# Optimization experiments

Measured on AMD Instinct MI355X. Metric: run time of the kernel, lower is better.

Reference implementation:

```python
import jax, jax.numpy as jnp
import numpy as np

B, S, D = 2, 2048, 2048      # batch, seq, hidden_dim
F = 4096                      # expert ffn dim
E, K = 8, 2                   # num_experts, top_k


def setup_inputs() -> dict:
    key = jax.random.key(0)
    k0, k1, k2, k3, k4 = jax.random.split(key, 5)
    sc_d = 1.0 / np.sqrt(D)
    sc_f = 1.0 / np.sqrt(F)
    return {
        "hidden_states": jax.random.normal(k0, (B, S, D), jnp.float32),
        "gate_w": jax.random.normal(k1, (E, D), jnp.float32) * sc_d,  # router Linear(D->E)
        "w1": jax.random.normal(k2, (E, F, D), jnp.float32) * sc_d,   # stacked expert w1
        "w2": jax.random.normal(k3, (E, D, F), jnp.float32) * sc_f,   # stacked expert w2
        "w3": jax.random.normal(k4, (E, F, D), jnp.float32) * sc_d,   # stacked expert w3
    }


def reference(hidden_states, gate_w, w1, w2, w3):
    b, s, d = hidden_states.shape
    x = hidden_states.reshape(-1, d)                    # [T, D]
    T = x.shape[0]

    # Router: softmax in float32, top-k, renormalize (matches torch code)
    logits = x @ gate_w.T                               # [T, E]
    probs = jax.nn.softmax(logits.astype(jnp.float32), axis=-1)
    top_w, top_e = jax.lax.top_k(probs, K)              # [T, K]
    top_w = top_w / jnp.sum(top_w, axis=-1, keepdims=True)
    top_w = top_w.astype(x.dtype)

    # Scatter top-k weights into dense per-expert weight matrix [T, E]
    rows = jnp.arange(T)[:, None]
    w_full = jnp.zeros((T, E), x.dtype).at[rows, top_e].set(top_w)

    # Expert SwiGLU MLPs; dense-per-expert with zero weight for unrouted tokens
    # is mathematically identical to the gather/scatter loop in the original.
    y = jnp.zeros_like(x)
    for e in range(E):
        h = jax.nn.silu(x @ w1[e].T) * (x @ w3[e].T)    # [T, F]
        y = y + w_full[:, e:e + 1] * (h @ w2[e].T)      # [T, D]

    return y.reshape(b, s, d)
```

## Files before the change

kernel.cpp:

```cpp
#include <hip/hip_runtime.h>
#include <hip/hip_bf16.h>

#define TTOK 4096
#define DIM  2048
#define FF   4096
#define NE   8
#define TROWS 8192

#define BM 256
#define BK 64

typedef __attribute__((ext_vector_type(4))) float  f32x4;
typedef __attribute__((ext_vector_type(8))) short  s16x8;
typedef __attribute__((ext_vector_type(8))) unsigned short u16x8;

__device__ __forceinline__ unsigned short f2bf(float f) {
  union { __hip_bfloat16 h; unsigned short u; } cv;
  cv.h = __float2bfloat16(f);
  return cv.u;
}
__device__ __forceinline__ float bf2f(unsigned short u) {
  union { unsigned int i; float f; } cv;
  cv.i = ((unsigned int)u) << 16;
  return cv.f;
}

__device__ __forceinline__ void gl_lds16(const void* g, void* s) {
  __builtin_amdgcn_global_load_lds(
      (__attribute__((address_space(1))) void*)(g),
      (__attribute__((address_space(3))) void*)(s), 16, 0, 0);
}

#define VMW(NN) asm volatile("s_waitcnt vmcnt(" #NN ")" ::: "memory")

__global__ __launch_bounds__(256) void cvt_kernel(const float* __restrict__ s,
                                                  unsigned short* __restrict__ d, int n8) {
  int i = blockIdx.x * 256 + threadIdx.x;
  if (i >= n8) return;
  f32x4 v0 = *(const f32x4*)(s + (size_t)i * 8);
  f32x4 v1 = *(const f32x4*)(s + (size_t)i * 8 + 4);
  u16x8 o;
#pragma unroll
  for (int j = 0; j < 4; ++j) { o[j] = f2bf(v0[j]); o[j + 4] = f2bf(v1[j]); }
  *(u16x8*)(d + (size_t)i * 8) = o;
}

__global__ void router_kernel(const float* __restrict__ x,
                              const float* __restrict__ gate_w,
                              int* __restrict__ tope, float* __restrict__ topw,
                              int* __restrict__ counts) {
  const int t = blockIdx.x;
  const int tid = threadIdx.x;
  const float* xr = x + (size_t)t * DIM;
  float p[NE];
#pragma unroll
  for (int e = 0; e < NE; ++e) p[e] = 0.f;
  for (int d = tid; d < DIM; d += 256) {
    float xv = xr[d];
#pragma unroll
    for (int e = 0; e < NE; ++e) p[e] += xv * gate_w[e * DIM + d];
  }
#pragma unroll
  for (int off = 32; off > 0; off >>= 1) {
#pragma unroll
    for (int e = 0; e < NE; ++e) p[e] += __shfl_down(p[e], off);
  }
  __shared__ float red[4][NE];
  const int wid = tid >> 6, lane = tid & 63;
  if (lane == 0) {
#pragma unroll
    for (int e = 0; e < NE; ++e) red[wid][e] = p[e];
  }
  __syncthreads();
  if (tid == 0) {
    float l[NE];
#pragma unroll
    for (int e = 0; e < NE; ++e) l[e] = red[0][e] + red[1][e] + red[2][e] + red[3][e];
    float mx = l[0];
#pragma unroll
    for (int e = 1; e < NE; ++e) mx = fmaxf(mx, l[e]);
    float pr[NE]; float sum = 0.f;
#pragma unroll
    for (int e = 0; e < NE; ++e) { pr[e] = __expf(l[e] - mx); sum += pr[e]; }
    float inv = 1.f / sum;
#pragma unroll
    for (int e = 0; e < NE; ++e) pr[e] *= inv;
    int i0 = 0; float p0 = pr[0];
#pragma unroll
    for (int e = 1; e < NE; ++e) if (pr[e] > p0) { p0 = pr[e]; i0 = e; }
    int i1 = -1; float p1 = -1.f;
#pragma unroll
    for (int e = 0; e < NE; ++e) if (e != i0 && pr[e] > p1) { p1 = pr[e]; i1 = e; }
    float wsum = p0 + p1;
    tope[t * 2 + 0] = i0; topw[t * 2 + 0] = p0 / wsum;
    tope[t * 2 + 1] = i1; topw[t * 2 + 1] = p1 / wsum;
    atomicAdd(&counts[i0], 1);
    atomicAdd(&counts[i1], 1);
  }
}

__global__ void prefix_kernel(const int* __restrict__ counts, int* __restrict__ basep) {
  if (threadIdx.x == 0 && blockIdx.x == 0) {
    int acc = 0;
    for (int e = 0; e < NE; ++e) { basep[e] = acc; acc += counts[e]; }
  }
}

__global__ void fill_kernel(const int* __restrict__ tope, const float* __restrict__ topw,
                            const int* __restrict__ basep, int* __restrict__ fillp,
                            int* __restrict__ rowtok, float* __restrict__ roww,
                            int* __restrict__ rowof) {
  int t = blockIdx.x * blockDim.x + threadIdx.x;
  if (t >= TTOK) return;
#pragma unroll
  for (int s = 0; s < 2; ++s) {
    int e = tope[t * 2 + s];
    int r = basep[e] + atomicAdd(&fillp[e], 1);
    rowtok[r] = t;
    roww[r] = topw[t * 2 + s];
    rowof[t * 2 + s] = r;
  }
}

template <int MODE, int K, int N>
__global__ __launch_bounds__(512, 1) void gemm8(
    const unsigned short* __restrict__ Asrc, const unsigned short* __restrict__ Bw,
    const int* __restrict__ rowtok, const float* __restrict__ roww,
    const int* __restrict__ counts, const int* __restrict__ basep,
    void* __restrict__ Out) {
  const int e = blockIdx.z;
  const int cnt = counts[e];
  const int m0 = blockIdx.y * BM;
  if (m0 >= cnt) return;
  const int n0 = blockIdx.x * BM;
  const int base_e = basep[e];

  __shared__ unsigned short As[2][BM * BK];
  __shared__ unsigned short Bs[2][BM * BK];

  const int tid = threadIdx.x;
  const int lane = tid & 63;
  const int w = tid >> 6;
  const int wm = w >> 2;
  const int wn = w & 3;

  const int lsub  = lane >> 3;
  const int lslot = lane & 7;
  const int swz_e = 8 * (lslot ^ lsub);

  const unsigned short* pA[4];
  const unsigned short* pB[4];
#pragma unroll
  for (int s = 0; s < 4; ++s) {
    int rl = s * 64 + w * 8 + lsub;
    int ga = m0 + rl; if (ga > cnt - 1) ga = cnt - 1;
    if (MODE == 0) {
      int tok = rowtok[base_e + ga];
      pA[s] = Asrc + (size_t)tok * K + swz_e;
    } else {
      pA[s] = Asrc + (size_t)(base_e + ga) * K + swz_e;
    }
    pB[s] = Bw + ((size_t)e * N + n0 + s * 64 + w * 8 + lsub) * K + swz_e;
  }

  const int frow = lane & 15;
  const int klane = lane >> 4;
  const int ks0 = (klane * 8) ^ ((frow & 7) * 8);
  const int ks1 = (32 + klane * 8) ^ ((frow & 7) * 8);

  f32x4 acc[8][4];
#pragma unroll
  for (int mf = 0; mf < 8; ++mf)
#pragma unroll
    for (int nf = 0; nf < 4; ++nf) acc[mf][nf] = (f32x4)0.f;

#define ST_A(BUF, G0, T) do { \
    gl_lds16(pA[G0]     + (size_t)(T) * BK, &As[BUF][((G0) * 64 + w * 8) * BK]); \
    gl_lds16(pA[(G0)+1] + (size_t)(T) * BK, &As[BUF][(((G0)+1) * 64 + w * 8) * BK]); \
  } while (0)
#define ST_B(BUF, G0, T) do { \
    gl_lds16(pB[G0]     + (size_t)(T) * BK, &Bs[BUF][((G0) * 64 + w * 8) * BK]); \
    gl_lds16(pB[(G0)+1] + (size_t)(T) * BK, &Bs[BUF][(((G0)+1) * 64 + w * 8) * BK]); \
  } while (0)

#define RD_A(MH, BUF) do { \
    _Pragma("unroll") \
    for (int ii = 0; ii < 4; ++ii) { \
      a[ii][0] = *(const s16x8*)&As[BUF][(wm * 128 + (MH) * 64 + ii * 16 + frow) * BK + ks0]; \
      a[ii][1] = *(const s16x8*)&As[BUF][(wm * 128 + (MH) * 64 + ii * 16 + frow) * BK + ks1]; \
    } } while (0)
#define RD_B(DST, NH, BUF) do { \
    _Pragma("unroll") \
    for (int j = 0; j < 2; ++j) { \
      DST[j][0] = *(const s16x8*)&Bs[BUF][(wn * 64 + (NH) * 32 + j * 16 + frow) * BK + ks0]; \
      DST[j][1] = *(const s16x8*)&Bs[BUF][(wn * 64 + (NH) * 32 + j * 16 + frow) * BK + ks1]; \
    } } while (0)

#define MM(MH, NH, BB) do { \
    __builtin_amdgcn_s_setprio(1); \
    _Pragma("unroll") \
    for (int ii = 0; ii < 4; ++ii) \
      _Pragma("unroll") \
      for (int j = 0; j < 2; ++j) { \
        acc[(MH) * 4 + ii][(NH) * 2 + j] = __builtin_amdgcn_mfma_f32_16x16x32_bf16( \
            a[ii][0], BB[j][0], acc[(MH) * 4 + ii][(NH) * 2 + j], 0, 0, 0); \
        acc[(MH) * 4 + ii][(NH) * 2 + j] = __builtin_amdgcn_mfma_f32_16x16x32_bf16( \
            a[ii][1], BB[j][1], acc[(MH) * 4 + ii][(NH) * 2 + j], 0, 0, 0); \
      } \
    __builtin_amdgcn_s_setprio(0); \
  } while (0)

#define MIDSYNC do { \
    __builtin_amdgcn_sched_barrier(0); \
    __builtin_amdgcn_s_barrier(); \
    asm volatile("s_waitcnt lgkmcnt(0)" ::: "memory"); \
    __builtin_amdgcn_sched_barrier(0); \
  } while (0)
#define ENDB do { \
    __builtin_amdgcn_sched_barrier(0); \
    __builtin_amdgcn_s_barrier(); \
  } while (0)

  const int NT = K / BK;

  ST_A(0, 0, 0); ST_A(0, 2, 0);
  ST_B(0, 0, 0); ST_B(0, 2, 0);
  ST_B(1, 0, 1); ST_B(1, 2, 1);
  VMW(4);
  __builtin_amdgcn_s_barrier();

  s16x8 a[4][2], bl[2][2], bh[2][2];

  for (int t = 0; t < NT; t += 2) {
    const bool full = (t + 2 < NT);

    RD_A(0, 0); RD_B(bl, 0, 0);
    ST_A(1, 0, t + 1);
    MIDSYNC; MM(0, 0, bl); ENDB;

    RD_B(bh, 1, 0);
    ST_A(1, 2, t + 1);
    MIDSYNC; MM(0, 1, bh); ENDB;

    RD_A(1, 0);
    if (full) ST_B(0, 0, t + 2);
    MIDSYNC; MM(1, 1, bh); ENDB;

    if (full) ST_B(0, 2, t + 2);
    MIDSYNC; MM(1, 0, bl);
    if (full) { VMW(4); } else { VMW(0); }
    ENDB;

    RD_A(0, 1); RD_B(bl, 0, 1);
    if (full) ST_A(0, 0, t + 2);
    MIDSYNC; MM(0, 0, bl); ENDB;

    RD_B(bh, 1, 1);
    if (full) ST_A(0, 2, t + 2);
    MIDSYNC; MM(0, 1, bh); ENDB;

    RD_A(1, 1);
    if (full) ST_B(1, 0, t + 3);
    MIDSYNC; MM(1, 1, bh); ENDB;

    if (full) ST_B(1, 2, t + 3);
    MIDSYNC; MM(1, 0, bl);
    if (full) { VMW(4); }
    ENDB;
  }
#undef ST_A
#undef ST_B
#undef RD_A
#undef RD_B
#undef MM
#undef MIDSYNC
#undef ENDB

#pragma unroll
  for (int mf = 0; mf < 8; ++mf) {
#pragma unroll
    for (int nf = 0; nf < 4; ++nf) {
      int col = n0 + wn * 64 + nf * 16 + frow;
#pragma unroll
      for (int j = 0; j < 4; ++j) {
        int rl = wm * 128 + (mf >> 2) * 64 + (mf & 3) * 16 + klane * 4 + j;
        int grow = m0 + rl;
        if (grow < cnt) {
          if (MODE == 0) {
            ((unsigned short*)Out)[(size_t)(base_e + grow) * N + col] = f2bf(acc[mf][nf][j]);
          } else {
            float wv = roww[base_e + grow];
            ((float*)Out)[(size_t)(base_e + grow) * N + col] = acc[mf][nf][j] * wv;
          }
        }
      }
    }
  }
}

__global__ __launch_bounds__(256) void swiglu_kernel(const unsigned short* __restrict__ h1,
                                                     const unsigned short* __restrict__ h3,
                                                     unsigned short* __restrict__ H, int n8) {
  int i = blockIdx.x * 256 + threadIdx.x;
  if (i >= n8) return;
  u16x8 v1 = *(const u16x8*)(h1 + (size_t)i * 8);
  u16x8 v3 = *(const u16x8*)(h3 + (size_t)i * 8);
  u16x8 o;
#pragma unroll
  for (int j = 0; j < 8; ++j) {
    float s = bf2f(v1[j]);
    float g = bf2f(v3[j]);
    o[j] = f2bf((s / (1.f + __expf(-s))) * g);
  }
  *(u16x8*)(H + (size_t)i * 8) = o;
}

__global__ __launch_bounds__(256) void combine_kernel(const float* __restrict__ R,
                                                      const int* __restrict__ rowof,
                                                      float* __restrict__ y) {
  int idx = blockIdx.x * 256 + threadIdx.x;
  int t = idx >> 9;
  int d4 = idx & 511;
  int r0 = rowof[t * 2], r1 = rowof[t * 2 + 1];
  f32x4 a = *(const f32x4*)(R + (size_t)r0 * DIM + d4 * 4);
  f32x4 b = *(const f32x4*)(R + (size_t)r1 * DIM + d4 * 4);
  *(f32x4*)(y + (size_t)t * DIM + d4 * 4) = a + b;
}

extern "C" void kernel_launch(void* const* d_in, const int* in_sizes, int n_in,
                              void* d_out, int out_size, void* d_ws, size_t ws_size,
                              hipStream_t stream) {
  const float* x      = (const float*)d_in[0];
  const float* gate_w = (const float*)d_in[1];
  const float* w1     = (const float*)d_in[2];
  const float* w2     = (const float*)d_in[3];
  const float* w3     = (const float*)d_in[4];
  float* y = (float*)d_out;

  char* ws = (char*)d_ws;
  const size_t MB = 1ull << 20;
  int*   tope   = (int*)(ws);
  float* topw   = (float*)(ws + (32 << 10));
  int*   rowtok = (int*)(ws + (64 << 10));
  float* roww   = (float*)(ws + (96 << 10));
  int*   rowof  = (int*)(ws + (128 << 10));
  int*   counts = (int*)(ws + (160 << 10));
  int*   basep  = counts + 32;
  int*   fillp  = counts + 64;

  unsigned short* xb  = (unsigned short*)(ws + 1 * MB);
  unsigned short* H1  = (unsigned short*)(ws + 17 * MB);
  unsigned short* H3  = (unsigned short*)(ws + 81 * MB);
  unsigned short* w1b = (unsigned short*)(ws + 145 * MB);
  unsigned short* w3b = (unsigned short*)(ws + 273 * MB);
  unsigned short* w2b = (unsigned short*)(ws + 401 * MB);
  float*          R   = (float*)(ws + 145 * MB);

  hipMemsetAsync(counts, 0, 512, stream);
  router_kernel<<<TTOK, 256, 0, stream>>>(x, gate_w, tope, topw, counts);
  prefix_kernel<<<1, 64, 0, stream>>>(counts, basep);
  fill_kernel<<<TTOK / 256, 256, 0, stream>>>(tope, topw, basep, fillp, rowtok, roww, rowof);

  const int nw8 = NE * FF * DIM / 8;
  const int nx8 = TTOK * DIM / 8;
  cvt_kernel<<<nw8 / 256, 256, 0, stream>>>(w1, w1b, nw8);
  cvt_kernel<<<nw8 / 256, 256, 0, stream>>>(w3, w3b, nw8);
  cvt_kernel<<<nw8 / 256, 256, 0, stream>>>(w2, w2b, nw8);
  cvt_kernel<<<nx8 / 256, 256, 0, stream>>>(x, xb, nx8);

  gemm8<0, DIM, FF><<<dim3(FF / BM, 16, NE), 512, 0, stream>>>(
      xb, w1b, rowtok, roww, counts, basep, (void*)H1);
  gemm8<0, DIM, FF><<<dim3(FF / BM, 16, NE), 512, 0, stream>>>(
      xb, w3b, rowtok, roww, counts, basep, (void*)H3);
  swiglu_kernel<<<TROWS * FF / 8 / 256, 256, 0, stream>>>(H1, H3, H1, TROWS * FF / 8);
  gemm8<1, FF, DIM><<<dim3(DIM / BM, 16, NE), 512, 0, stream>>>(
      H1, w2b, rowtok, roww, counts, basep, (void*)R);
  combine_kernel<<<TTOK * DIM / 4 / 256, 256, 0, stream>>>(R, rowof, y);
}
```

Measured before the change: 986.4 us.

## Fuse w1/w3 GEMMs with SwiGLU epilogue and remap workgroups across experts

Replaces the two separate up-projection GEMMs and the standalone SwiGLU kernel with one kernel. It loads a shared A tile once, computes both w1 and w3 accumulators over 128-wide N tiles, and applies SiLU*gate in the epilogue. This removes the H3 intermediate write/read and re-reading the gathered activations twice. It also adds a block-index remapping that interleaves experts across consecutive workgroups to balance load, at the cost of a narrower N tile per block.

```diff
diff --git a/kernel.cpp b/kernel.cpp
--- a/kernel.cpp
+++ b/kernel.cpp
@@ -32,6 +32,17 @@
 }
 
 #define VMW(NN) asm volatile("s_waitcnt vmcnt(" #NN ")" ::: "memory")
+
+#define MIDSYNC do { \
+    __builtin_amdgcn_sched_barrier(0); \
+    __builtin_amdgcn_s_barrier(); \
+    asm volatile("s_waitcnt lgkmcnt(0)" ::: "memory"); \
+    __builtin_amdgcn_sched_barrier(0); \
+  } while (0)
+#define ENDB do { \
+    __builtin_amdgcn_sched_barrier(0); \
+    __builtin_amdgcn_s_barrier(); \
+  } while (0)
 
 __global__ __launch_bounds__(256) void cvt_kernel(const float* __restrict__ s,
                                                   unsigned short* __restrict__ d, int n8) {
@@ -122,21 +133,28 @@
   }
 }
 
-template <int MODE, int K, int N>
-__global__ __launch_bounds__(512, 1) void gemm8(
-    const unsigned short* __restrict__ Asrc, const unsigned short* __restrict__ Bw,
-    const int* __restrict__ rowtok, const float* __restrict__ roww,
+__global__ __launch_bounds__(512, 1) void gemm1f(
+    const unsigned short* __restrict__ xb, const unsigned short* __restrict__ w1b,
+    const unsigned short* __restrict__ w3b, const int* __restrict__ rowtok,
     const int* __restrict__ counts, const int* __restrict__ basep,
-    void* __restrict__ Out) {
-  const int e = blockIdx.z;
+    unsigned short* __restrict__ H) {
+  constexpr int GX = FF / 128;
+  constexpr int GY = TTOK / BM;
+  constexpr int Q  = GX * GY;
+  int lin = (blockIdx.z * GY + blockIdx.y) * GX + blockIdx.x;
+  int wg = (lin & 7) * Q + (lin >> 3);
+  const int e   = wg / (GX * GY);
+  const int rem = wg % (GX * GY);
+  const int m0  = (rem / GX) * BM;
+  const int n0  = (rem % GX) * 128;
+
   const int cnt = counts[e];
-  const int m0 = blockIdx.y * BM;
   if (m0 >= cnt) return;
-  const int n0 = blockIdx.x * BM;
   const int base_e = basep[e];
 
   __shared__ unsigned short As[2][BM * BK];
-  __shared__ unsigned short Bs[2][BM * BK];
+  __shared__ unsigned short B1s[2][128 * BK];
+  __shared__ unsigned short B3s[2][128 * BK];
 
   const int tid = threadIdx.x;
   const int lane = tid & 63;
@@ -149,18 +167,181 @@
   const int swz_e = 8 * (lslot ^ lsub);
 
   const unsigned short* pA[4];
-  const unsigned short* pB[4];
+  const unsigned short* pB1[2];
+  const unsigned short* pB3[2];
 #pragma unroll
   for (int s = 0; s < 4; ++s) {
     int rl = s * 64 + w * 8 + lsub;
     int ga = m0 + rl; if (ga > cnt - 1) ga = cnt - 1;
-    if (MODE == 0) {
-      int tok = rowtok[base_e + ga];
-      pA[s] = Asrc + (size_t)tok * K + swz_e;
-    } else {
-      pA[s] = Asrc + (size_t)(base_e + ga) * K + swz_e;
+    int tok = rowtok[base_e + ga];
+    pA[s] = xb + (size_t)tok * DIM + swz_e;
+  }
+#pragma unroll
+  for (int s = 0; s < 2; ++s) {
+    int rl = s * 64 + w * 8 + lsub;
+    pB1[s] = w1b + ((size_t)e * FF + n0 + rl) * DIM + swz_e;
+    pB3[s] = w3b + ((size_t)e * FF + n0 + rl) * DIM + swz_e;
+  }
+
+  const int frow = lane & 15;
+  const int klane = lane >> 4;
+  const int ks0 = (klane * 8) ^ ((frow & 7) * 8);
+  const int ks1 = (32 + klane * 8) ^ ((frow & 7) * 8);
+
+  f32x4 acc1[8][2], acc3[8][2];
+#pragma unroll
+  for (int mf = 0; mf < 8; ++mf)
+#pragma unroll
+    for (int nf = 0; nf < 2; ++nf) { acc1[mf][nf] = (f32x4)0.f; acc3[mf][nf] = (f32x4)0.f; }
+
+#define ST_A(BUF, G0, T) do { \
+    gl_lds16(pA[G0]     + (size_t)(T) * BK, &As[BUF][((G0) * 64 + w * 8) * BK]); \
+    gl_lds16(pA[(G0)+1] + (size_t)(T) * BK, &As[BUF][(((G0)+1) * 64 + w * 8) * BK]); \
+  } while (0)
+#define ST_B1(BUF, T) do { \
+    gl_lds16(pB1[0] + (size_t)(T) * BK, &B1s[BUF][(0  + w * 8) * BK]); \
+    gl_lds16(pB1[1] + (size_t)(T) * BK, &B1s[BUF][(64 + w * 8) * BK]); \
+  } while (0)
+#define ST_B3(BUF, T) do { \
+    gl_lds16(pB3[0] + (size_t)(T) * BK, &B3s[BUF][(0  + w * 8) * BK]); \
+    gl_lds16(pB3[1] + (size_t)(T) * BK, &B3s[BUF][(64 + w * 8) * BK]); \
+  } while (0)
+
+#define RD_A(MH, BUF) do { \
+    _Pragma("unroll") \
+    for (int ii = 0; ii < 4; ++ii) { \
+      a[ii][0] = *(const s16x8*)&As[BUF][(wm * 128 + (MH) * 64 + ii * 16 + frow) * BK + ks0]; \
+      a[ii][1] = *(const s16x8*)&As[BUF][(wm * 128 + (MH) * 64 + ii * 16 + frow) * BK + ks1]; \
+    } } while (0)
+#define RD_BX(DST, ARR, BUF) do { \
+    _Pragma("unroll") \
+    for (int j = 0; j < 2; ++j) { \
+      DST[j][0] = *(const s16x8*)&ARR[BUF][(wn * 32 + j * 16 + frow) * BK + ks0]; \
+      DST[j][1] = *(const s16x8*)&ARR[BUF][(wn * 32 + j * 16 + frow) * BK + ks1]; \
+    } } while (0)
+
+#define MMX(ACC, MH, BB) do { \
+    __builtin_amdgcn_s_setprio(1); \
+    _Pragma("unroll") \
+    for (int ii = 0; ii < 4; ++ii) \
+      _Pragma("unroll") \
+      for (int j = 0; j < 2; ++j) { \
+        ACC[(MH) * 4 + ii][j] = __builtin_amdgcn_mfma_f32_16x16x32_bf16( \
+            a[ii][0], BB[j][0], ACC[(MH) * 4 + ii][j], 0, 0, 0); \
+        ACC[(MH) * 4 + ii][j] = __builtin_amdgcn_mfma_f32_16x16x32_bf16( \
+            a[ii][1], BB[j][1], ACC[(MH) * 4 + ii][j], 0, 0, 0); \
+      } \
+    __builtin_amdgcn_s_setprio(0); \
+  } while (0)
+
+  const int NT = DIM / BK;
+
+  ST_A(0, 0, 0); ST_A(0, 2, 0);
+  ST_B1(0, 0); ST_B3(0, 0);
+  ST_B1(1, 1); ST_B3(1, 1);
+  VMW(4);
+  __builtin_amdgcn_s_barrier();
+
+  s16x8 a[4][2], bl[2][2], bh[2][2];
+
+  for (int t = 0; t < NT; t += 2) {
+    const bool full = (t + 2 < NT);
+
+    RD_A(0, 0); RD_BX(bl, B1s, 0);
+    ST_A(1, 0, t + 1);
+    MIDSYNC; MMX(acc1, 0, bl); ENDB;
+    RD_BX(bh, B3s, 0);
+    ST_A(1, 2, t + 1);
+    MIDSYNC; MMX(acc3, 0, bh); ENDB;
+    RD_A(1, 0);
+    if (full) ST_B1(0, t + 2);
+    MIDSYNC; MMX(acc3, 1, bh); ENDB;
+    if (full) ST_B3(0, t + 2);
+    MIDSYNC; MMX(acc1, 1, bl);
+    if (full) { VMW(4); } else { VMW(0); }
+    ENDB;
+
+    RD_A(0, 1); RD_BX(bl, B1s, 1);
+    if (full) ST_A(0, 0, t + 2);
+    MIDSYNC; MMX(acc1, 0, bl); ENDB;
+    RD_BX(bh, B3s, 1);
+    if (full) ST_A(0, 2, t + 2);
+    MIDSYNC; MMX(acc3, 0, bh); ENDB;
+    RD_A(1, 1);
+    if (full) ST_B1(1, t + 3);
+    MIDSYNC; MMX(acc3, 1, bh); ENDB;
+    if (full) ST_B3(1, t + 3);
+    MIDSYNC; MMX(acc1, 1, bl);
+    if (full) { VMW(4); }
+    ENDB;
+  }
+#undef ST_A
+#undef ST_B1
+#undef ST_B3
+#undef RD_A
+#undef RD_BX
+#undef MMX
+
+#pragma unroll
+  for (int mf = 0; mf < 8; ++mf) {
+#pragma unroll
+    for (int nf = 0; nf < 2; ++nf) {
+      int col = n0 + wn * 32 + nf * 16 + frow;
+      f32x4 c1 = acc1[mf][nf], c3 = acc3[mf][nf];
+#pragma unroll
+      for (int j = 0; j < 4; ++j) {
+        int rl = wm * 128 + (mf >> 2) * 64 + (mf & 3) * 16 + klane * 4 + j;
+        int grow = m0 + rl;
+        if (grow < cnt) {
+          float s = c1[j];
+          float hval = (s / (1.f + __expf(-s))) * c3[j];
+          H[(size_t)(base_e + grow) * FF + col] = f2bf(hval);
+        }
+      }
     }
-    pB[s] = Bw + ((size_t)e * N + n0 + s * 64 + w * 8 + lsub) * K + swz_e;
+  }
+}
+
+template <int K, int N>
+__global__ __launch_bounds__(512, 1) void gemm8(
+    const unsigned short* __restrict__ Asrc, const unsigned short* __restrict__ Bw,
+    const float* __restrict__ roww, const int* __restrict__ counts,
+    const int* __restrict__ basep, float* __restrict__ Out) {
+  constexpr int GX = N / BM;
+  constexpr int GY = TTOK / BM;
+  constexpr int Q  = GX * GY;
+  int lin = (blockIdx.z * GY + blockIdx.y) * GX + blockIdx.x;
+  int wg = (lin & 7) * Q + (lin >> 3);
+  const int e   = wg / (GX * GY);
+  const int rem = wg % (GX * GY);
+  const int m0  = (rem / GX) * BM;
+  const int n0  = (rem % GX) * BM;
+
+  const int cnt = counts[e];
+  if (m0 >= cnt) return;
+  const int base_e = basep[e];
+
+  __shared__ unsigned short As[2][BM * BK];
+  __shared__ unsigned short Bs[2][BM * BK];
+
+  const int tid = threadIdx.x;
+  const int lane = tid & 63;
+  const int w = tid >> 6;
+  const int wm = w >> 2;
+  const int wn = w & 3;
+
+  const int lsub  = lane >> 3;
+  const int lslot = lane & 7;
+  const int swz_e = 8 * (lslot ^ lsub);
+
+  const unsigned short* pA[4];
+  const unsigned short* pB[4];
+#pragma unroll
+  for (int s = 0; s < 4; ++s) {
+    int rl = s * 64 + w * 8 + lsub;
+    int ga = m0 + rl; if (ga > cnt - 1) ga = cnt - 1;
+    pA[s] = Asrc + (size_t)(base_e + ga) * K + swz_e;
+    pB[s] = Bw + ((size_t)e * N + n0 + rl) * K + swz_e;
   }
 
   const int frow = lane & 15;
@@ -210,17 +391,6 @@
     __builtin_amdgcn_s_setprio(0); \
   } while (0)
 
-#define MIDSYNC do { \
-    __builtin_amdgcn_sched_barrier(0); \
-    __builtin_amdgcn_s_barrier(); \
-    asm volatile("s_waitcnt lgkmcnt(0)" ::: "memory"); \
-    __builtin_amdgcn_sched_barrier(0); \
-  } while (0)
-#define ENDB do { \
-    __builtin_amdgcn_sched_barrier(0); \
-    __builtin_amdgcn_s_barrier(); \
-  } while (0)
-
   const int NT = K / BK;
 
   ST_A(0, 0, 0); ST_A(0, 2, 0);
@@ -273,8 +443,6 @@
 #undef RD_A
 #undef RD_B
 #undef MM
-#undef MIDSYNC
-#undef ENDB
 
 #pragma unroll
   for (int mf = 0; mf < 8; ++mf) {
@@ -286,33 +454,12 @@
         int rl = wm * 128 + (mf >> 2) * 64 + (mf & 3) * 16 + klane * 4 + j;
         int grow = m0 + rl;
         if (grow < cnt) {
-          if (MODE == 0) {
-            ((unsigned short*)Out)[(size_t)(base_e + grow) * N + col] = f2bf(acc[mf][nf][j]);
-          } else {
-            float wv = roww[base_e + grow];
-            ((float*)Out)[(size_t)(base_e + grow) * N + col] = acc[mf][nf][j] * wv;
-          }
+          float wv = roww[base_e + grow];
+          Out[(size_t)(base_e + grow) * N + col] = acc[mf][nf][j] * wv;
         }
       }
     }
   }
-}
-
-__global__ __launch_bounds__(256) void swiglu_kernel(const unsigned short* __restrict__ h1,
-                                                     const unsigned short* __restrict__ h3,
-                                                     unsigned short* __restrict__ H, int n8) {
-  int i = blockIdx.x * 256 + threadIdx.x;
-  if (i >= n8) return;
-  u16x8 v1 = *(const u16x8*)(h1 + (size_t)i * 8);
-  u16x8 v3 = *(const u16x8*)(h3 + (size_t)i * 8);
-  u16x8 o;
-#pragma unroll
-  for (int j = 0; j < 8; ++j) {
-    float s = bf2f(v1[j]);
-    float g = bf2f(v3[j]);
-    o[j] = f2bf((s / (1.f + __expf(-s))) * g);
-  }
-  *(u16x8*)(H + (size_t)i * 8) = o;
 }
 
 __global__ __launch_bounds__(256) void combine_kernel(const float* __restrict__ R,
@@ -350,11 +497,10 @@
 
   unsigned short* xb  = (unsigned short*)(ws + 1 * MB);
   unsigned short* H1  = (unsigned short*)(ws + 17 * MB);
-  unsigned short* H3  = (unsigned short*)(ws + 81 * MB);
   unsigned short* w1b = (unsigned short*)(ws + 145 * MB);
   unsigned short* w3b = (unsigned short*)(ws + 273 * MB);
   unsigned short* w2b = (unsigned short*)(ws + 401 * MB);
-  float*          R   = (float*)(ws + 145 * MB);
+  float*          R   = (float*)(ws + 81 * MB);
 
   hipMemsetAsync(counts, 0, 512, stream);
   router_kernel<<<TTOK, 256, 0, stream>>>(x, gate_w, tope, topw, counts);
@@ -368,12 +514,9 @@
   cvt_kernel<<<nw8 / 256, 256, 0, stream>>>(w2, w2b, nw8);
   cvt_kernel<<<nx8 / 256, 256, 0, stream>>>(x, xb, nx8);
 
-  gemm8<0, DIM, FF><<<dim3(FF / BM, 16, NE), 512, 0, stream>>>(
-      xb, w1b, rowtok, roww, counts, basep, (void*)H1);
-  gemm8<0, DIM, FF><<<dim3(FF / BM, 16, NE), 512, 0, stream>>>(
-      xb, w3b, rowtok, roww, counts, basep, (void*)H3);
-  swiglu_kernel<<<TROWS * FF / 8 / 256, 256, 0, stream>>>(H1, H3, H1, TROWS * FF / 8);
-  gemm8<1, FF, DIM><<<dim3(DIM / BM, 16, NE), 512, 0, stream>>>(
-      H1, w2b, rowtok, roww, counts, basep, (void*)R);
+  gemm1f<<<dim3(FF / 128, TTOK / BM, NE), 512, 0, stream>>>(
+      xb, w1b, w3b, rowtok, counts, basep, H1);
+  gemm8<FF, DIM><<<dim3(DIM / BM, TTOK / BM, NE), 512, 0, stream>>>(
+      H1, w2b, roww, counts, basep, R);
   combine_kernel<<<TTOK * DIM / 4 / 256, 256, 0, stream>>>(R, rowof, y);
 }
```

New measurement: 968.5 us. No clear change (-1.8%).
